# Optimization experiments

Hardware: AMD Instinct MI355X
Metric: run time of the kernel (lower is better)

The kernel has to match this reference:

```python
import jax, jax.numpy as jnp
import numpy as np

BN_EPS = 1e-3  # Keras BatchNormalization default epsilon


def setup_inputs() -> dict:
    key = jax.random.key(0)
    ks = jax.random.split(key, 10)
    B, H, W, F, K = 16, 64, 64, 512, 32
    support = 1.0 / np.sqrt(K * F)
    fc_support = np.sqrt(1.0 / F)
    return {
        "inputs": jax.random.normal(ks[0], (B, H, W, F), dtype=jnp.float32),
        # Encoder params
        "codewords": jax.random.uniform(ks[1], (K, F), minval=-support, maxval=support, dtype=jnp.float32),
        "smoothing": jax.random.uniform(ks[2], (K,), minval=-1.0, maxval=0.0, dtype=jnp.float32),
        # BatchNorm (inference mode: moving stats) over feature axis of (B, K, F)
        "bn_gamma": jnp.ones((F,), dtype=jnp.float32),
        "bn_beta": jnp.zeros((F,), dtype=jnp.float32),
        "bn_mean": jnp.zeros((F,), dtype=jnp.float32),
        "bn_var": jnp.ones((F,), dtype=jnp.float32),
        # Dense layers
        "fc_enc_w": jax.random.uniform(ks[3], (F, F), minval=-fc_support, maxval=fc_support, dtype=jnp.float32),
        "fc_enc_b": jax.random.uniform(ks[4], (F,), minval=-fc_support, maxval=fc_support, dtype=jnp.float32),
        "fc_se_w": jax.random.uniform(ks[5], (F, 1), minval=-fc_support, maxval=fc_support, dtype=jnp.float32),
        "fc_se_b": jax.random.uniform(ks[6], (1,), minval=-fc_support, maxval=fc_support, dtype=jnp.float32),
    }


def _encoder(x, codewords, smoothing, bn_gamma, bn_beta, bn_mean, bn_var):
    # x: (B, H, W, F) -> feats (B, N, F)
    B, H, W, F = x.shape
    feats = x.reshape(B, H * W, F)
    # Squared residual norms without materializing (B, N, K, F):
    x2 = jnp.sum(feats * feats, axis=-1, keepdims=True)          # (B, N, 1)
    c2 = jnp.sum(codewords * codewords, axis=-1)                 # (K,)
    xc = jnp.einsum("bnf,kf->bnk", feats, codewords)             # (B, N, K)
    sqnorms = x2 - 2.0 * xc + c2                                 # (B, N, K)
    s = jax.nn.softmax(sqnorms * smoothing, axis=-1)             # (B, N, K)
    # sum_n s[b,n,k] * (x[b,n] - c[k]) = s^T x - c * sum_n s
    s_sum = jnp.sum(s, axis=1)                                   # (B, K)
    enc = jnp.einsum("bnk,bnf->bkf", s, feats) - s_sum[:, :, None] * codewords  # (B, K, F)
    # BatchNorm (inference) + ReLU, then aggregate over codewords
    enc_bn = (enc - bn_mean) * jax.lax.rsqrt(bn_var + BN_EPS) * bn_gamma + bn_beta
    return jnp.sum(jax.nn.relu(enc_bn), axis=1)                  # (B, F)


def reference(inputs, codewords, smoothing, bn_gamma, bn_beta, bn_mean, bn_var,
              fc_enc_w, fc_enc_b, fc_se_w, fc_se_b):
    enc = _encoder(inputs, codewords, smoothing, bn_gamma, bn_beta, bn_mean, bn_var)
    attn = jax.nn.sigmoid(enc @ fc_enc_w + fc_enc_b)             # (B, F)
    featuremaps_out = attn[:, None, None, :] * inputs            # (B, H, W, F)
    se_loss_out = enc @ fc_se_w + fc_se_b                        # (B, 1)
    return (featuremaps_out, se_loss_out)
```

## Files before the change

### kernel.cpp

```cpp
#include <hip/hip_runtime.h>
#include <hip/hip_bf16.h>
#include <math.h>

#define Bb   16
#define HWn  4096
#define Ff   512
#define Kk   32
#define GCH  32

typedef __attribute__((ext_vector_type(8))) short  short8;
typedef __attribute__((ext_vector_type(4))) float  f32x4;

#define WS_SSUM  0
#define WS_EOUT  512
#define WS_ATTN  (WS_EOUT + Bb * Ff)
#define WS_CWB   (WS_ATTN + Bb * Ff)
#define WS_C2    (WS_CWB + 8192)
#define WS_SM    (WS_C2 + 32)

#define SCR_PART 0
#define SCR_RED  16777216

static __device__ __forceinline__ unsigned int pack2bf(float a, float b) {
    union { __hip_bfloat162 h; unsigned int u; } p;
    p.h = __float22bfloat162_rn(make_float2(a, b));
    return p.u;
}

__global__ void prep(const float* __restrict__ cw, const float* __restrict__ smth,
                     unsigned short* __restrict__ cwb,
                     float* __restrict__ c2l2, float* __restrict__ sml2)
{
    const int t = threadIdx.x;
    const float4* c4 = (const float4*)cw;
    #pragma unroll
    for (int j = 0; j < 16; ++j) {
        const int i = t + j * 256;
        const float4 v = c4[i];
        *reinterpret_cast<uint2*>(&cwb[i * 4]) =
            make_uint2(pack2bf(v.x, v.y), pack2bf(v.z, v.w));
    }
    const int k = t >> 3, sk = t & 7;
    float p = 0.f;
    #pragma unroll
    for (int j = 0; j < 16; ++j) {
        const float4 v = c4[k * 128 + sk + j * 8];
        p = fmaf(v.x, v.x, fmaf(v.y, v.y, fmaf(v.z, v.z, fmaf(v.w, v.w, p))));
    }
    p += __shfl_xor(p, 1); p += __shfl_xor(p, 2); p += __shfl_xor(p, 4);
    if (sk == 0) {
        const float L2E = 1.4426950408889634f;
        const float sm = smth[k];
        sml2[k] = sm * L2E;
        c2l2[k] = p * sm * L2E;
    }
}

__global__ __launch_bounds__(512, 2) void enc_fused(
    const float* __restrict__ x, const unsigned short* __restrict__ cwb,
    const float* __restrict__ c2l2, const float* __restrict__ sml2,
    float* __restrict__ part, float* __restrict__ s_sum)
{
    __shared__ __align__(16) float s_lds[128 * 32];
    __shared__ float sm_s[32], c2_s[32];
    __shared__ float swred[8][32];

    const int tid  = threadIdx.x;
    const int wave = tid >> 6, lane = tid & 63;
    const int col  = lane & 15, g = lane >> 4;
    const int b    = blockIdx.y, cx = blockIdx.x;
    const int n_loc = wave * 16 + col;
    const int n     = cx * 128 + n_loc;

    if (tid < 32) { sm_s[tid] = sml2[tid]; c2_s[tid] = c2l2[tid]; }
    __syncthreads();

    {
        const float4* xr = (const float4*)(x + ((size_t)b * HWn + n) * Ff) + g * 2;
        const unsigned short* a0p = cwb + col * 512 + g * 8;
        const unsigned short* a1p = a0p + 16 * 512;
        f32x4 c0 = {0.f, 0.f, 0.f, 0.f}, c1 = {0.f, 0.f, 0.f, 0.f};
        float px = 0.f;
        #pragma unroll
        for (int fs = 0; fs < 16; ++fs) {
            const float4 v0 = xr[fs * 8];
            const float4 v1 = xr[fs * 8 + 1];
            px = fmaf(v0.x, v0.x, fmaf(v0.y, v0.y, fmaf(v0.z, v0.z, fmaf(v0.w, v0.w, px))));
            px = fmaf(v1.x, v1.x, fmaf(v1.y, v1.y, fmaf(v1.z, v1.z, fmaf(v1.w, v1.w, px))));
            union { uint4 u; short8 s; } bu;
            bu.u = make_uint4(pack2bf(v0.x, v0.y), pack2bf(v0.z, v0.w),
                              pack2bf(v1.x, v1.y), pack2bf(v1.z, v1.w));
            const short8 a0 = *(const short8*)(a0p + fs * 32);
            const short8 a1 = *(const short8*)(a1p + fs * 32);
            c0 = __builtin_amdgcn_mfma_f32_16x16x32_bf16(a0, bu.s, c0, 0, 0, 0);
            c1 = __builtin_amdgcn_mfma_f32_16x16x32_bf16(a1, bu.s, c1, 0, 0, 0);
        }
        px += __shfl_xor(px, 16); px += __shfl_xor(px, 32);

        float lg[8];
        #pragma unroll
        for (int r = 0; r < 4; ++r) {
            const int k0 = g * 4 + r;
            lg[r]     = fmaf(sm_s[k0],      fmaf(-2.f, c0[r], px), c2_s[k0]);
            lg[4 + r] = fmaf(sm_s[k0 + 16], fmaf(-2.f, c1[r], px), c2_s[k0 + 16]);
        }
        float m = lg[0];
        #pragma unroll
        for (int j = 1; j < 8; ++j) m = fmaxf(m, lg[j]);
        m = fmaxf(m, __shfl_xor(m, 16)); m = fmaxf(m, __shfl_xor(m, 32));
        float e[8], sum = 0.f;
        #pragma unroll
        for (int j = 0; j < 8; ++j) { e[j] = exp2f(lg[j] - m); sum += e[j]; }
        sum += __shfl_xor(sum, 16); sum += __shfl_xor(sum, 32);
        const float inv = 1.f / sum;
        #pragma unroll
        for (int j = 0; j < 8; ++j) e[j] *= inv;

        #pragma unroll
        for (int r = 0; r < 4; ++r) {
            s_lds[n_loc * 32 + g * 4 + r]      = e[r];
            s_lds[n_loc * 32 + 16 + g * 4 + r] = e[4 + r];
        }
        #pragma unroll
        for (int j = 0; j < 8; ++j) {
            float v = e[j];
            v += __shfl_xor(v, 1); v += __shfl_xor(v, 2);
            v += __shfl_xor(v, 4); v += __shfl_xor(v, 8);
            if (col == 0) swred[wave][((j & 4) << 2) + g * 4 + (j & 3)] = v;
        }
    }
    __syncthreads();
    if (tid < 32) {
        float a = 0.f;
        #pragma unroll
        for (int w = 0; w < 8; ++w) a += swred[w][tid];
        atomicAdd(&s_sum[b * Kk + tid], a);
    }

    float acc[4][8];
    #pragma unroll
    for (int j = 0; j < 4; ++j)
        #pragma unroll
        for (int i = 0; i < 8; ++i) acc[j][i] = 0.f;

    const int kq = wave * 4;
    const float4* xp = (const float4*)(x + ((size_t)b * HWn + cx * 128) * Ff) + lane * 2;
    #pragma unroll 4
    for (int nn = 0; nn < 128; ++nn) {
        const f32x4 sv = *(const f32x4*)&s_lds[nn * 32 + kq];
        const float4 v0 = xp[nn * 128];
        const float4 v1 = xp[nn * 128 + 1];
        const float fx[8] = {v0.x, v0.y, v0.z, v0.w, v1.x, v1.y, v1.z, v1.w};
        #pragma unroll
        for (int j = 0; j < 4; ++j) {
            const float sj = sv[j];
            #pragma unroll
            for (int i = 0; i < 8; ++i)
                acc[j][i] = fmaf(sj, fx[i], acc[j][i]);
        }
    }
    float* basep = part + (size_t)(b * GCH + cx) * (Kk * Ff) +
                   (size_t)(wave * 4) * Ff + lane * 8;
    #pragma unroll
    for (int j = 0; j < 4; ++j) {
        *reinterpret_cast<float4*>(basep + j * Ff) =
            make_float4(acc[j][0], acc[j][1], acc[j][2], acc[j][3]);
        *reinterpret_cast<float4*>(basep + j * Ff + 4) =
            make_float4(acc[j][4], acc[j][5], acc[j][6], acc[j][7]);
    }
}

__global__ void enc_red(const float* __restrict__ scr, float* __restrict__ outp)
{
    const int idx = blockIdx.x * 256 + threadIdx.x;
    const int b   = idx >> 14;
    const int rem = idx & 16383;
    const float* p = scr + (size_t)b * GCH * 16384 + rem;
    float a = 0.f;
    #pragma unroll
    for (int c = 0; c < GCH; ++c) a += p[c * 16384];
    outp[idx] = a;
}

__global__ void enc_finish(const float* __restrict__ enc_acc,
                           const float* __restrict__ s_sum,
                           const float* __restrict__ cw,
                           const float* __restrict__ gamma,
                           const float* __restrict__ beta,
                           const float* __restrict__ mean,
                           const float* __restrict__ var,
                           const float* __restrict__ se_w,
                           const float* __restrict__ se_b,
                           float* __restrict__ enc_out,
                           float* __restrict__ se_out)
{
    __shared__ float ss[Kk];
    __shared__ float red[8];
    const int b = blockIdx.x, f = threadIdx.x;
    if (f < Kk) ss[f] = s_sum[b * Kk + f];
    __syncthreads();
    const float m  = mean[f];
    const float g  = gamma[f];
    const float bt = beta[f];
    const float iv = rsqrtf(var[f] + 1e-3f);
    float a = 0.f;
    #pragma unroll 4
    for (int k = 0; k < Kk; ++k) {
        float v = enc_acc[((long)b * Kk + k) * Ff + f] - ss[k] * cw[k * Ff + f];
        v = (v - m) * iv * g + bt;
        a += fmaxf(v, 0.f);
    }
    enc_out[b * Ff + f] = a;
    float p = a * se_w[f];
    p += __shfl_down(p, 32); p += __shfl_down(p, 16); p += __shfl_down(p, 8);
    p += __shfl_down(p, 4);  p += __shfl_down(p, 2);  p += __shfl_down(p, 1);
    if ((f & 63) == 0) red[f >> 6] = p;
    __syncthreads();
    if (f == 0) {
        float t = 0.f;
        #pragma unroll
        for (int i = 0; i < 8; ++i) t += red[i];
        se_out[b] = t + se_b[0];
    }
}

__global__ void attn_fc(const float* __restrict__ enc_out,
                        const float* __restrict__ W,
                        const float* __restrict__ bias,
                        float* __restrict__ attn)
{
    __shared__ float eo[Bb][Ff];
    const int t = threadIdx.x, fg = blockIdx.x;
    #pragma unroll
    for (int j = 0; j < 4; ++j)
        reinterpret_cast<float4*>(&eo[0][0])[t + j * 512] =
            reinterpret_cast<const float4*>(enc_out)[t + j * 512];
    __syncthreads();
    const int f  = fg * 64 + (t & 63);
    const int b0 = t >> 6;
    float a0 = bias[f], a1 = bias[f];
    #pragma unroll 8
    for (int fp = 0; fp < Ff; ++fp) {
        const float w = W[fp * Ff + f];
        a0 = fmaf(eo[b0][fp],     w, a0);
        a1 = fmaf(eo[b0 + 8][fp], w, a1);
    }
    attn[b0 * Ff + f]       = 1.f / (1.f + expf(-a0));
    attn[(b0 + 8) * Ff + f] = 1.f / (1.f + expf(-a1));
}

__global__ void bcast_mul(const float4* __restrict__ x4,
                          const float* __restrict__ attn,
                          float4* __restrict__ o4)
{
    const int stride = gridDim.x * blockDim.x;
    const int total4 = Bb * HWn * Ff / 4;
    for (int i = blockIdx.x * blockDim.x + threadIdx.x; i < total4; i += stride) {
        const float4 v = x4[i];
        const int f4 = i & 127;
        const int bb = i >> 19;
        const float4 a = *reinterpret_cast<const float4*>(&attn[bb * Ff + f4 * 4]);
        o4[i] = make_float4(v.x * a.x, v.y * a.y, v.z * a.z, v.w * a.w);
    }
}

extern "C" void kernel_launch(void* const* d_in, const int* in_sizes, int n_in,
                              void* d_out, int out_size, void* d_ws, size_t ws_size,
                              hipStream_t stream)
{
    (void)in_sizes; (void)n_in; (void)out_size; (void)ws_size;
    const float* x     = (const float*)d_in[0];
    const float* cw    = (const float*)d_in[1];
    const float* smth  = (const float*)d_in[2];
    const float* gamma = (const float*)d_in[3];
    const float* beta  = (const float*)d_in[4];
    const float* mean  = (const float*)d_in[5];
    const float* var   = (const float*)d_in[6];
    const float* Wenc  = (const float*)d_in[7];
    const float* benc  = (const float*)d_in[8];
    const float* Wse   = (const float*)d_in[9];
    const float* bse   = (const float*)d_in[10];

    float* out = (float*)d_out;
    float* ws  = (float*)d_ws;
    float* ssum = ws + WS_SSUM;
    float* eout = ws + WS_EOUT;
    float* attn = ws + WS_ATTN;
    unsigned short* cwb = (unsigned short*)(ws + WS_CWB);
    float* c2l2 = ws + WS_C2;
    float* sml2 = ws + WS_SM;

    float* scr_part = out + SCR_PART;
    float* scr_red  = out + SCR_RED;

    hipMemsetAsync(ssum, 0, (size_t)Bb * Kk * sizeof(float), stream);
    prep<<<1, 256, 0, stream>>>(cw, smth, cwb, c2l2, sml2);
    enc_fused<<<dim3(GCH, Bb), 512, 0, stream>>>(x, cwb, c2l2, sml2, scr_part, ssum);
    enc_red<<<1024, 256, 0, stream>>>(scr_part, scr_red);
    enc_finish<<<Bb, 512, 0, stream>>>(scr_red, ssum, cw, gamma, beta, mean, var,
                                       Wse, bse, eout, out + (long)Bb * HWn * Ff);
    attn_fc<<<8, 512, 0, stream>>>(eout, Wenc, benc, attn);
    bcast_mul<<<2048, 256, 0, stream>>>((const float4*)x, attn, (float4*)out);
}
```

Baseline: 175.0 us.

## Halve rows per block, split feature dim across wave pairs, restructure softmax

The encoder block now processes 64 spatial rows instead of 128, doubling the grid (GCH 64). Each pair of waves splits the 512-feature dot product in half and writes partial x·c and ||x||² to LDS, where a separate pass sums them and computes the softmax with 8 threads per row. This raises block count and parallelism to help latency hiding. The cost is an extra LDS round trip and barrier, and twice as many partial sums to reduce later.

```diff
diff --git a/kernel.cpp b/kernel.cpp
--- a/kernel.cpp
+++ b/kernel.cpp
@@ -6,7 +6,7 @@
 #define HWn  4096
 #define Ff   512
 #define Kk   32
-#define GCH  32
+#define GCH  64
 
 typedef __attribute__((ext_vector_type(8))) short  short8;
 typedef __attribute__((ext_vector_type(4))) float  f32x4;
@@ -61,7 +61,8 @@
     const float* __restrict__ c2l2, const float* __restrict__ sml2,
     float* __restrict__ part, float* __restrict__ s_sum)
 {
-    __shared__ __align__(16) float s_lds[128 * 32];
+    __shared__ __align__(16) float lgp[2][64][32];
+    __shared__ float x2p[2][64];
     __shared__ float sm_s[32], c2_s[32];
     __shared__ float swred[8][32];
 
@@ -69,20 +70,20 @@
     const int wave = tid >> 6, lane = tid & 63;
     const int col  = lane & 15, g = lane >> 4;
     const int b    = blockIdx.y, cx = blockIdx.x;
-    const int n_loc = wave * 16 + col;
-    const int n     = cx * 128 + n_loc;
+    const int gr   = wave >> 1, fh = wave & 1;
+    const int n_loc = gr * 16 + col;
+    const int n     = cx * 64 + n_loc;
 
     if (tid < 32) { sm_s[tid] = sml2[tid]; c2_s[tid] = c2l2[tid]; }
-    __syncthreads();
 
     {
-        const float4* xr = (const float4*)(x + ((size_t)b * HWn + n) * Ff) + g * 2;
-        const unsigned short* a0p = cwb + col * 512 + g * 8;
+        const float4* xr = (const float4*)(x + ((size_t)b * HWn + n) * Ff) + fh * 64 + g * 2;
+        const unsigned short* a0p = cwb + col * 512 + fh * 256 + g * 8;
         const unsigned short* a1p = a0p + 16 * 512;
         f32x4 c0 = {0.f, 0.f, 0.f, 0.f}, c1 = {0.f, 0.f, 0.f, 0.f};
         float px = 0.f;
         #pragma unroll
-        for (int fs = 0; fs < 16; ++fs) {
+        for (int fs = 0; fs < 8; ++fs) {
             const float4 v0 = xr[fs * 8];
             const float4 v1 = xr[fs * 8 + 1];
             px = fmaf(v0.x, v0.x, fmaf(v0.y, v0.y, fmaf(v0.z, v0.z, fmaf(v0.w, v0.w, px))));
@@ -96,38 +97,47 @@
             c1 = __builtin_amdgcn_mfma_f32_16x16x32_bf16(a1, bu.s, c1, 0, 0, 0);
         }
         px += __shfl_xor(px, 16); px += __shfl_xor(px, 32);
-
-        float lg[8];
+        if (g == 0) x2p[fh][n_loc] = px;
         #pragma unroll
         for (int r = 0; r < 4; ++r) {
-            const int k0 = g * 4 + r;
-            lg[r]     = fmaf(sm_s[k0],      fmaf(-2.f, c0[r], px), c2_s[k0]);
-            lg[4 + r] = fmaf(sm_s[k0 + 16], fmaf(-2.f, c1[r], px), c2_s[k0 + 16]);
-        }
-        float m = lg[0];
-        #pragma unroll
-        for (int j = 1; j < 8; ++j) m = fmaxf(m, lg[j]);
-        m = fmaxf(m, __shfl_xor(m, 16)); m = fmaxf(m, __shfl_xor(m, 32));
-        float e[8], sum = 0.f;
-        #pragma unroll
-        for (int j = 0; j < 8; ++j) { e[j] = exp2f(lg[j] - m); sum += e[j]; }
-        sum += __shfl_xor(sum, 16); sum += __shfl_xor(sum, 32);
+            lgp[fh][n_loc][g * 4 + r]      = c0[r];
+            lgp[fh][n_loc][16 + g * 4 + r] = c1[r];
+        }
+    }
+    __syncthreads();
+
+    const int srow = tid >> 3, sf = tid & 7;
+    float ssl[4];
+    {
+        const float x2v = x2p[0][srow] + x2p[1][srow];
+        float lg[4];
+        #pragma unroll
+        for (int r = 0; r < 4; ++r) {
+            const int k = sf * 4 + r;
+            const float xc = lgp[0][srow][k] + lgp[1][srow][k];
+            lg[r] = fmaf(sm_s[k], fmaf(-2.f, xc, x2v), c2_s[k]);
+        }
+        float m = fmaxf(fmaxf(lg[0], lg[1]), fmaxf(lg[2], lg[3]));
+        m = fmaxf(m, __shfl_xor(m, 1));
+        m = fmaxf(m, __shfl_xor(m, 2));
+        m = fmaxf(m, __shfl_xor(m, 4));
+        float e[4], sum = 0.f;
+        #pragma unroll
+        for (int r = 0; r < 4; ++r) { e[r] = exp2f(lg[r] - m); sum += e[r]; }
+        sum += __shfl_xor(sum, 1); sum += __shfl_xor(sum, 2); sum += __shfl_xor(sum, 4);
         const float inv = 1.f / sum;
         #pragma unroll
-        for (int j = 0; j < 8; ++j) e[j] *= inv;
-
-        #pragma unroll
         for (int r = 0; r < 4; ++r) {
-            s_lds[n_loc * 32 + g * 4 + r]      = e[r];
-            s_lds[n_loc * 32 + 16 + g * 4 + r] = e[4 + r];
-        }
-        #pragma unroll
-        for (int j = 0; j < 8; ++j) {
-            float v = e[j];
-            v += __shfl_xor(v, 1); v += __shfl_xor(v, 2);
-            v += __shfl_xor(v, 4); v += __shfl_xor(v, 8);
-            if (col == 0) swred[wave][((j & 4) << 2) + g * 4 + (j & 3)] = v;
-        }
+            const float s = e[r] * inv;
+            lgp[0][srow][sf * 4 + r] = s;
+            ssl[r] = s;
+        }
+    }
+    #pragma unroll
+    for (int r = 0; r < 4; ++r) {
+        float v = ssl[r];
+        v += __shfl_xor(v, 8); v += __shfl_xor(v, 16); v += __shfl_xor(v, 32);
+        if (lane < 8) swred[wave][lane * 4 + r] = v;
     }
     __syncthreads();
     if (tid < 32) {
@@ -144,10 +154,11 @@
         for (int i = 0; i < 8; ++i) acc[j][i] = 0.f;
 
     const int kq = wave * 4;
-    const float4* xp = (const float4*)(x + ((size_t)b * HWn + cx * 128) * Ff) + lane * 2;
+    const float* s_base = &lgp[0][0][0];
+    const float4* xp = (const float4*)(x + ((size_t)b * HWn + cx * 64) * Ff) + lane * 2;
     #pragma unroll 4
-    for (int nn = 0; nn < 128; ++nn) {
-        const f32x4 sv = *(const f32x4*)&s_lds[nn * 32 + kq];
+    for (int nn = 0; nn < 64; ++nn) {
+        const f32x4 sv = *(const f32x4*)&s_base[nn * 32 + kq];
         const float4 v0 = xp[nn * 128];
         const float4 v1 = xp[nn * 128 + 1];
         const float fx[8] = {v0.x, v0.y, v0.z, v0.w, v1.x, v1.y, v1.z, v1.w};
```

Measured after the change: 191.5 us. 9.5% more time.
